# Kernel optimization log

Measured on AMD Instinct MI355X. Metric: run time of the kernel, lower is better.

The kernel has to match this reference:

```python
import jax, jax.numpy as jnp
import numpy as np

NUM_TOKENS = 8192
SEQ_LEN = 128
BATCH = 8192
INIT_SCALE = 0.02


def setup_inputs() -> dict:
    key = jax.random.key(0)
    k1, k2, k3, k4 = jax.random.split(key, 4)
    return {
        "rx_real": jax.random.normal(k1, (BATCH, SEQ_LEN), dtype=jnp.float32),
        "rx_imag": jax.random.normal(k2, (BATCH, SEQ_LEN), dtype=jnp.float32),
        "freq_real": jax.random.normal(k3, (NUM_TOKENS, SEQ_LEN), dtype=jnp.float32) * INIT_SCALE,
        "freq_imag": jax.random.normal(k4, (NUM_TOKENS, SEQ_LEN), dtype=jnp.float32) * INIT_SCALE,
        "temperature": jnp.asarray(1.0, dtype=jnp.float32),
    }


def reference(rx_real, rx_imag, freq_real, freq_imag, temperature):
    # Build complex waveform bank: ifft of learned frequency-domain params (ortho norm)
    freq = freq_real + 1j * freq_imag                      # [T, L] complex64
    bank = jnp.fft.ifft(freq, axis=-1, norm="ortho")       # [T, L] complex64

    rx = rx_real + 1j * rx_imag                            # [B, L] complex64

    # 'dot' similarity: complex GEMM against conjugated bank, then squared magnitude
    score = rx @ jnp.conj(bank).T                          # [B, T] complex64
    sim = score.real ** 2 + score.imag ** 2                # [B, T] float32

    # temperature scaling (use_temperature=True)
    return sim / temperature
```

## Files before the change

kernel.cpp:

```cpp
#include <hip/hip_runtime.h>
#include <stdint.h>


#define T_TOKENS 8192
#define B_BATCH  8192
#define L_SEQ    128
#define KDIM     256

typedef __bf16 bf16x8 __attribute__((ext_vector_type(8)));
typedef float  f32x4  __attribute__((ext_vector_type(4)));
typedef unsigned int u32x4 __attribute__((ext_vector_type(4)));

__device__ __forceinline__ unsigned short f2bf(float f) {
  unsigned int u = __builtin_bit_cast(unsigned int, f);
  u += 0x7FFFu + ((u >> 16) & 1u);
  return (unsigned short)(u >> 16);
}

__global__ void build_bank_kernel(const float* __restrict__ fr,
                                  const float* __restrict__ fi,
                                  unsigned int* __restrict__ B2) {
  __shared__ float  sfr[L_SEQ], sfi[L_SEQ];
  __shared__ float2 stw[L_SEQ];
  const int t = blockIdx.x, l = threadIdx.x;
  sfr[l] = fr[t * L_SEQ + l];
  sfi[l] = fi[t * L_SEQ + l];
  float sn, cs;
  __sincosf(6.283185307179586f * (float)l * (1.0f / 128.0f), &sn, &cs);
  stw[l] = make_float2(cs, sn);
  __syncthreads();
  float br = 0.f, bi = 0.f;
#pragma unroll 8
  for (int k = 0; k < L_SEQ; ++k) {
    const float2 tw = stw[(k * l) & 127];
    const float xr = sfr[k], xi = sfi[k];
    br = fmaf(xr, tw.x, br); br = fmaf(-xi, tw.y, br);
    bi = fmaf(xr, tw.y, bi); bi = fmaf(xi, tw.x, bi);
  }
  const float sc = 0.08838834764831845f;
  const unsigned int lo = f2bf(br * sc);
  const unsigned int hi = f2bf(bi * sc);
  B2[t * L_SEQ + l] = lo | (hi << 16);
}

__global__ void build_a_kernel(const float* __restrict__ rr,
                               const float* __restrict__ ri,
                               unsigned int* __restrict__ A2) {
  const int i = blockIdx.x * 256 + threadIdx.x;
  const unsigned int lo = f2bf(rr[i]);
  const unsigned int hi = f2bf(ri[i]);
  A2[i] = lo | (hi << 16);
}

typedef const __attribute__((address_space(1))) unsigned int* gas_u32p;
typedef __attribute__((address_space(3))) unsigned int* las_u32p;

__device__ __forceinline__ void gl_lds16(const void* g, void* l) {
  __builtin_amdgcn_global_load_lds((gas_u32p)g, (las_u32p)l, 16, 0, 0);
}

__device__ __forceinline__ bf16x8 make_imag(bf16x8 a) {
  u32x4 u = __builtin_bit_cast(u32x4, a);
#pragma unroll
  for (int i = 0; i < 4; ++i)
    u[i] = ((u[i] >> 16) | (u[i] << 16)) ^ 0x80000000u;
  return __builtin_bit_cast(bf16x8, u);
}

__global__ __launch_bounds__(256, 2) void gemm_kernel(
    const unsigned short* __restrict__ A2,
    const unsigned short* __restrict__ B2,
    const float* __restrict__ temp,
    float* __restrict__ out) {
  __shared__ __align__(16) unsigned short sA[2][128 * 64];
  __shared__ __align__(16) unsigned short sB[2][128 * 64];

  const int tid  = threadIdx.x;
  const int lane = tid & 63;
  const int wid  = tid >> 6;

  const int bid  = blockIdx.x;
  const int swz  = (bid & 7) * 512 + (bid >> 3);
  const int brow = swz >> 6;
  const int bcol = swz & 63;
  const int wr = wid >> 1, wc = wid & 1;

  const unsigned short* Abase = A2 + (size_t)brow * 128 * KDIM;
  const unsigned short* Bbase = B2 + (size_t)bcol * 128 * KDIM;

  f32x4 accre[4][4], accim[4][4];
#pragma unroll
  for (int m = 0; m < 4; ++m)
#pragma unroll
    for (int n = 0; n < 4; ++n) {
      accre[m][n] = f32x4{0.f, 0.f, 0.f, 0.f};
      accim[m][n] = f32x4{0.f, 0.f, 0.f, 0.f};
    }

  auto stage = [&](int ks, int buf) {
#pragma unroll
    for (int q = 0; q < 4; ++q) {
      const int unit = (q * 4 + wid) * 64 + lane;
      const int r = unit >> 3;
      const int c = (unit & 7) << 3;
      gl_lds16(Abase + (size_t)r * KDIM + ks * 64 + c,
               (char*)&sA[buf][0] + (size_t)(q * 4 + wid) * 1024);
      gl_lds16(Bbase + (size_t)r * KDIM + ks * 64 + c,
               (char*)&sB[buf][0] + (size_t)(q * 4 + wid) * 1024);
    }
  };

  stage(0, 0);

#pragma unroll
  for (int ks = 0; ks < 4; ++ks) {
    const int buf = ks & 1;
    __syncthreads();
    if (ks < 3) stage(ks + 1, buf ^ 1);

    const unsigned short* aptr =
        &sA[buf][(wr * 64 + (lane & 15)) * 64 + ((lane >> 4) << 3)];
    const unsigned short* bptr =
        &sB[buf][(wc * 64 + (lane & 15)) * 64 + ((lane >> 4) << 3)];
#pragma unroll
    for (int kk = 0; kk < 2; ++kk) {
      bf16x8 a[4], b[4];
#pragma unroll
      for (int m = 0; m < 4; ++m)
        a[m] = *(const bf16x8*)(aptr + m * 16 * 64 + kk * 32);
#pragma unroll
      for (int n = 0; n < 4; ++n)
        b[n] = *(const bf16x8*)(bptr + n * 16 * 64 + kk * 32);
#pragma unroll
      for (int m = 0; m < 4; ++m) {
        const bf16x8 ai = make_imag(a[m]);
#pragma unroll
        for (int n = 0; n < 4; ++n) {
          accre[m][n] = __builtin_amdgcn_mfma_f32_16x16x32_bf16(
              a[m], b[n], accre[m][n], 0, 0, 0);
          accim[m][n] = __builtin_amdgcn_mfma_f32_16x16x32_bf16(
              ai, b[n], accim[m][n], 0, 0, 0);
        }
      }
    }
  }

  const float inv_t = 1.0f / temp[0];
  const int r0 = brow * 128 + wr * 64 + ((lane >> 4) << 2);
  const int c0 = bcol * 128 + wc * 64 + (lane & 15);
#pragma unroll
  for (int m = 0; m < 4; ++m) {
#pragma unroll
    for (int n = 0; n < 4; ++n) {
      const f32x4 re = accre[m][n];
      const f32x4 im = accim[m][n];
#pragma unroll
      for (int j = 0; j < 4; ++j) {
        out[(size_t)(r0 + m * 16 + j) * T_TOKENS + (c0 + n * 16)] =
            (re[j] * re[j] + im[j] * im[j]) * inv_t;
      }
    }
  }
}

extern "C" void kernel_launch(void* const* d_in, const int* in_sizes, int n_in,
                              void* d_out, int out_size, void* d_ws, size_t ws_size,
                              hipStream_t stream) {
  const float* rx_r = (const float*)d_in[0];
  const float* rx_i = (const float*)d_in[1];
  const float* fq_r = (const float*)d_in[2];
  const float* fq_i = (const float*)d_in[3];
  const float* temp = (const float*)d_in[4];
  float* out = (float*)d_out;

  unsigned int* B2 = (unsigned int*)d_ws;
  unsigned int* A2 = (unsigned int*)((char*)d_ws + (4u << 20));

  build_bank_kernel<<<T_TOKENS, L_SEQ, 0, stream>>>(fq_r, fq_i, B2);
  build_a_kernel<<<(B_BATCH * L_SEQ) / 256, 256, 0, stream>>>(rx_r, rx_i, A2);
  gemm_kernel<<<(B_BATCH / 128) * (T_TOKENS / 128), 256, 0, stream>>>(
      (const unsigned short*)A2, (const unsigned short*)B2, temp, out);
}
```

Before: 123.9 us.

## Enlarge GEMM tile to 256x128 with 4-slot LDS pipeline and swizzle

```diff
diff --git a/kernel.cpp b/kernel.cpp
--- a/kernel.cpp
+++ b/kernel.cpp
@@ -5,7 +5,9 @@
 #define T_TOKENS 8192
 #define B_BATCH  8192
 #define L_SEQ    128
-#define KDIM     256
+
+#define SLOT_BYTES 24576
+#define SB_OFF     16384
 
 typedef __bf16 bf16x8 __attribute__((ext_vector_type(8)));
 typedef float  f32x4  __attribute__((ext_vector_type(4)));
@@ -52,11 +54,10 @@
   A2[i] = lo | (hi << 16);
 }
 
-typedef const __attribute__((address_space(1))) unsigned int* gas_u32p;
-typedef __attribute__((address_space(3))) unsigned int* las_u32p;
-
-__device__ __forceinline__ void gl_lds16(const void* g, void* l) {
-  __builtin_amdgcn_global_load_lds((gas_u32p)g, (las_u32p)l, 16, 0, 0);
+__device__ __forceinline__ void gl_lds16(const char* g, char* l) {
+  __builtin_amdgcn_global_load_lds(
+      (const __attribute__((address_space(1))) unsigned int*)g,
+      (__attribute__((address_space(3))) unsigned int*)l, 16, 0, 0);
 }
 
 __device__ __forceinline__ bf16x8 make_imag(bf16x8 a) {
@@ -67,26 +68,46 @@
   return __builtin_bit_cast(bf16x8, u);
 }
 
-__global__ __launch_bounds__(256, 2) void gemm_kernel(
-    const unsigned short* __restrict__ A2,
-    const unsigned short* __restrict__ B2,
-    const float* __restrict__ temp,
-    float* __restrict__ out) {
-  __shared__ __align__(16) unsigned short sA[2][128 * 64];
-  __shared__ __align__(16) unsigned short sB[2][128 * 64];
-
+__device__ __forceinline__ int swz4(int row) { return ((row + (row >> 2)) & 3) << 4; }
+
+extern __shared__ __align__(16) char smem[];
+
+__global__ __launch_bounds__(512, 1) void gemm_kernel(
+    const char* __restrict__ A2, const char* __restrict__ B2,
+    const float* __restrict__ temp, float* __restrict__ out) {
   const int tid  = threadIdx.x;
   const int lane = tid & 63;
   const int wid  = tid >> 6;
 
+  const float inv_t = 1.0f / temp[0];
+  asm volatile("" :: "v"(inv_t));
+
   const int bid  = blockIdx.x;
-  const int swz  = (bid & 7) * 512 + (bid >> 3);
+  const int swz  = (bid & 7) * 256 + (bid >> 3);
   const int brow = swz >> 6;
   const int bcol = swz & 63;
   const int wr = wid >> 1, wc = wid & 1;
 
-  const unsigned short* Abase = A2 + (size_t)brow * 128 * KDIM;
-  const unsigned short* Bbase = B2 + (size_t)bcol * 128 * KDIM;
+  const int l4 = lane >> 2, lm = lane & 3;
+  const int rowA0 = wid * 32 + l4;
+  const int rowA1 = rowA0 + 16;
+  const int rowB  = wid * 16 + l4;
+  const char* gA0 = A2 + (size_t)(brow * 256 + rowA0) * 512 + ((lm * 16) ^ swz4(rowA0));
+  const char* gA1 = A2 + (size_t)(brow * 256 + rowA1) * 512 + ((lm * 16) ^ swz4(rowA1));
+  const char* gB  = B2 + (size_t)(bcol * 128 + rowB ) * 512 + ((lm * 16) ^ swz4(rowB));
+
+  int offA[4], offB[4];
+  const int cb = (lane >> 4) * 16;
+#pragma unroll
+  for (int m = 0; m < 4; ++m) {
+    const int r = wr * 64 + m * 16 + (lane & 15);
+    offA[m] = r * 64 + (cb ^ swz4(r));
+  }
+#pragma unroll
+  for (int n = 0; n < 4; ++n) {
+    const int r = wc * 64 + n * 16 + (lane & 15);
+    offB[n] = SB_OFF + r * 64 + (cb ^ swz4(r));
+  }
 
   f32x4 accre[4][4], accim[4][4];
 #pragma unroll
@@ -97,56 +118,65 @@
       accim[m][n] = f32x4{0.f, 0.f, 0.f, 0.f};
     }
 
-  auto stage = [&](int ks, int buf) {
-#pragma unroll
-    for (int q = 0; q < 4; ++q) {
-      const int unit = (q * 4 + wid) * 64 + lane;
-      const int r = unit >> 3;
-      const int c = (unit & 7) << 3;
-      gl_lds16(Abase + (size_t)r * KDIM + ks * 64 + c,
-               (char*)&sA[buf][0] + (size_t)(q * 4 + wid) * 1024);
-      gl_lds16(Bbase + (size_t)r * KDIM + ks * 64 + c,
-               (char*)&sB[buf][0] + (size_t)(q * 4 + wid) * 1024);
-    }
-  };
-
-  stage(0, 0);
-
-#pragma unroll
-  for (int ks = 0; ks < 4; ++ks) {
-    const int buf = ks & 1;
-    __syncthreads();
-    if (ks < 3) stage(ks + 1, buf ^ 1);
-
-    const unsigned short* aptr =
-        &sA[buf][(wr * 64 + (lane & 15)) * 64 + ((lane >> 4) << 3)];
-    const unsigned short* bptr =
-        &sB[buf][(wc * 64 + (lane & 15)) * 64 + ((lane >> 4) << 3)];
-#pragma unroll
-    for (int kk = 0; kk < 2; ++kk) {
-      bf16x8 a[4], b[4];
-#pragma unroll
-      for (int m = 0; m < 4; ++m)
-        a[m] = *(const bf16x8*)(aptr + m * 16 * 64 + kk * 32);
-#pragma unroll
-      for (int n = 0; n < 4; ++n)
-        b[n] = *(const bf16x8*)(bptr + n * 16 * 64 + kk * 32);
-#pragma unroll
-      for (int m = 0; m < 4; ++m) {
-        const bf16x8 ai = make_imag(a[m]);
-#pragma unroll
-        for (int n = 0; n < 4; ++n) {
-          accre[m][n] = __builtin_amdgcn_mfma_f32_16x16x32_bf16(
-              a[m], b[n], accre[m][n], 0, 0, 0);
-          accim[m][n] = __builtin_amdgcn_mfma_f32_16x16x32_bf16(
-              ai, b[n], accim[m][n], 0, 0, 0);
-        }
-      }
-    }
-  }
-
-  const float inv_t = 1.0f / temp[0];
-  const int r0 = brow * 128 + wr * 64 + ((lane >> 4) << 2);
+#define STAGE(KC) do {                                                     \
+    char* sl_ = smem + ((KC) & 3) * SLOT_BYTES;                            \
+    int koff_ = (KC) * 64;                                                 \
+    asm("" : "+v"(koff_));                                                 \
+    gl_lds16(gA0 + koff_, sl_ + wid * 2048);                               \
+    gl_lds16(gA1 + koff_, sl_ + wid * 2048 + 1024);                        \
+    gl_lds16(gB  + koff_, sl_ + SB_OFF + wid * 1024);                      \
+  } while (0)
+
+#define FENCE asm volatile("" ::: "memory")
+
+#define PHASE(C, VM, DOSTAGE) do {                                         \
+    const char* slb_ = smem + ((C) & 3) * SLOT_BYTES;                      \
+    bf16x8 a_[4], b_[4];                                                   \
+    _Pragma("unroll") for (int m = 0; m < 4; ++m)                          \
+      a_[m] = *(const bf16x8*)(slb_ + offA[m]);                            \
+    _Pragma("unroll") for (int n = 0; n < 4; ++n)                          \
+      b_[n] = *(const bf16x8*)(slb_ + offB[n]);                            \
+    if (DOSTAGE) { STAGE((C) + 3); }                                       \
+    if ((VM) == 4)      asm volatile("s_waitcnt vmcnt(4)" ::: "memory");   \
+    else if ((VM) == 3) asm volatile("s_waitcnt vmcnt(3)" ::: "memory");   \
+    else if ((VM) == 0) asm volatile("s_waitcnt vmcnt(0)" ::: "memory");   \
+    __builtin_amdgcn_s_barrier();                                          \
+    asm volatile("s_waitcnt lgkmcnt(0)" ::: "memory");                     \
+    __builtin_amdgcn_s_setprio(1);                                         \
+    _Pragma("unroll") for (int m = 0; m < 4; ++m) {                        \
+      const bf16x8 ai_ = make_imag(a_[m]);                                 \
+      _Pragma("unroll") for (int n = 0; n < 4; ++n) {                      \
+        accre[m][n] = __builtin_amdgcn_mfma_f32_16x16x32_bf16(             \
+            a_[m], b_[n], accre[m][n], 0, 0, 0);                           \
+        accim[m][n] = __builtin_amdgcn_mfma_f32_16x16x32_bf16(             \
+            ai_, b_[n], accim[m][n], 0, 0, 0);                             \
+      }                                                                    \
+    }                                                                      \
+    __builtin_amdgcn_s_setprio(0);                                         \
+    __builtin_amdgcn_s_barrier();                                          \
+    FENCE;                                                                 \
+  } while (0)
+
+  asm volatile("s_waitcnt vmcnt(0) lgkmcnt(0)" ::: "memory");
+
+  STAGE(0); STAGE(1); STAGE(2);
+  asm volatile("s_waitcnt vmcnt(4)" ::: "memory");
+  __builtin_amdgcn_s_barrier();
+  FENCE;
+
+  PHASE(0, 4, 1);
+  PHASE(1, 4, 1);
+  PHASE(2, 4, 1);
+  PHASE(3, 4, 1);
+  PHASE(4, 4, 1);
+  PHASE(5, 3, 0);
+  PHASE(6, 0, 0);
+  PHASE(7, -1, 0);
+
+#undef PHASE
+#undef STAGE
+
+  const int r0 = brow * 256 + wr * 64 + ((lane >> 4) << 2);
   const int c0 = bcol * 128 + wc * 64 + (lane & 15);
 #pragma unroll
   for (int m = 0; m < 4; ++m) {
@@ -176,8 +206,11 @@
   unsigned int* B2 = (unsigned int*)d_ws;
   unsigned int* A2 = (unsigned int*)((char*)d_ws + (4u << 20));
 
+  (void)hipFuncSetAttribute((const void*)gemm_kernel,
+                            hipFuncAttributeMaxDynamicSharedMemorySize, 98304);
+
   build_bank_kernel<<<T_TOKENS, L_SEQ, 0, stream>>>(fq_r, fq_i, B2);
   build_a_kernel<<<(B_BATCH * L_SEQ) / 256, 256, 0, stream>>>(rx_r, rx_i, A2);
-  gemm_kernel<<<(B_BATCH / 128) * (T_TOKENS / 128), 256, 0, stream>>>(
-      (const unsigned short*)A2, (const unsigned short*)B2, temp, out);
-}
+  gemm_kernel<<<(B_BATCH / 256) * (T_TOKENS / 128), 512, 98304, stream>>>(
+      (const char*)A2, (const char*)B2, temp, out);
+}
```

New measurement: 130.3 us. 5.1% more time.

## Keep bank tile in registers and stream A rows directly without LDS

Applied to the files above, without the earlier changes.

```diff
diff --git a/kernel.cpp b/kernel.cpp
--- a/kernel.cpp
+++ b/kernel.cpp
@@ -5,7 +5,6 @@
 #define T_TOKENS 8192
 #define B_BATCH  8192
 #define L_SEQ    128
-#define KDIM     256
 
 typedef __bf16 bf16x8 __attribute__((ext_vector_type(8)));
 typedef float  f32x4  __attribute__((ext_vector_type(4)));
@@ -52,13 +51,6 @@
   A2[i] = lo | (hi << 16);
 }
 
-typedef const __attribute__((address_space(1))) unsigned int* gas_u32p;
-typedef __attribute__((address_space(3))) unsigned int* las_u32p;
-
-__device__ __forceinline__ void gl_lds16(const void* g, void* l) {
-  __builtin_amdgcn_global_load_lds((gas_u32p)g, (las_u32p)l, 16, 0, 0);
-}
-
 __device__ __forceinline__ bf16x8 make_imag(bf16x8 a) {
   u32x4 u = __builtin_bit_cast(u32x4, a);
 #pragma unroll
@@ -67,97 +59,91 @@
   return __builtin_bit_cast(bf16x8, u);
 }
 
-__global__ __launch_bounds__(256, 2) void gemm_kernel(
-    const unsigned short* __restrict__ A2,
-    const unsigned short* __restrict__ B2,
-    const float* __restrict__ temp,
-    float* __restrict__ out) {
-  __shared__ __align__(16) unsigned short sA[2][128 * 64];
-  __shared__ __align__(16) unsigned short sB[2][128 * 64];
-
+__global__ __launch_bounds__(256, 3) void gemm_kernel(
+    const char* __restrict__ A2, const char* __restrict__ B2,
+    const float* __restrict__ temp, float* __restrict__ out) {
   const int tid  = threadIdx.x;
   const int lane = tid & 63;
   const int wid  = tid >> 6;
+  const float inv_t = 1.0f / temp[0];
 
   const int bid  = blockIdx.x;
-  const int swz  = (bid & 7) * 512 + (bid >> 3);
-  const int brow = swz >> 6;
-  const int bcol = swz & 63;
-  const int wr = wid >> 1, wc = wid & 1;
+  const int g    = bid & 7;
+  const int nblk = bid >> 3;
 
-  const unsigned short* Abase = A2 + (size_t)brow * 128 * KDIM;
-  const unsigned short* Bbase = B2 + (size_t)bcol * 128 * KDIM;
+  const int lrow = lane & 15;
+  const int lk16 = (lane >> 4) * 16;
 
-  f32x4 accre[4][4], accim[4][4];
+  bf16x8 br[8][2];
+  {
+    const char* bb = B2 + (size_t)(nblk * 32 + lrow) * 512 + lk16;
 #pragma unroll
-  for (int m = 0; m < 4; ++m)
+    for (int kc = 0; kc < 8; ++kc) {
 #pragma unroll
-    for (int n = 0; n < 4; ++n) {
+      for (int n = 0; n < 2; ++n)
+        br[kc][n] = *(const bf16x8*)(bb + (size_t)n * 16 * 512 + kc * 64);
+    }
+  }
+
+  const size_t aoff0 = (size_t)lrow * 512 + lk16;
+  const size_t aoff1 = aoff0 + 16 * 512;
+  const char* pA = A2 + ((size_t)g * 1024 + wid * 32) * 512;
+
+  f32x4 accre[2][2], accim[2][2];
+#pragma unroll
+  for (int m = 0; m < 2; ++m)
+#pragma unroll
+    for (int n = 0; n < 2; ++n) {
       accre[m][n] = f32x4{0.f, 0.f, 0.f, 0.f};
       accim[m][n] = f32x4{0.f, 0.f, 0.f, 0.f};
     }
 
-  auto stage = [&](int ks, int buf) {
+  bf16x8 ar[4][2];
 #pragma unroll
-    for (int q = 0; q < 4; ++q) {
-      const int unit = (q * 4 + wid) * 64 + lane;
-      const int r = unit >> 3;
-      const int c = (unit & 7) << 3;
-      gl_lds16(Abase + (size_t)r * KDIM + ks * 64 + c,
-               (char*)&sA[buf][0] + (size_t)(q * 4 + wid) * 1024);
-      gl_lds16(Bbase + (size_t)r * KDIM + ks * 64 + c,
-               (char*)&sB[buf][0] + (size_t)(q * 4 + wid) * 1024);
-    }
-  };
-
-  stage(0, 0);
-
-#pragma unroll
-  for (int ks = 0; ks < 4; ++ks) {
-    const int buf = ks & 1;
-    __syncthreads();
-    if (ks < 3) stage(ks + 1, buf ^ 1);
-
-    const unsigned short* aptr =
-        &sA[buf][(wr * 64 + (lane & 15)) * 64 + ((lane >> 4) << 3)];
-    const unsigned short* bptr =
-        &sB[buf][(wc * 64 + (lane & 15)) * 64 + ((lane >> 4) << 3)];
-#pragma unroll
-    for (int kk = 0; kk < 2; ++kk) {
-      bf16x8 a[4], b[4];
-#pragma unroll
-      for (int m = 0; m < 4; ++m)
-        a[m] = *(const bf16x8*)(aptr + m * 16 * 64 + kk * 32);
-#pragma unroll
-      for (int n = 0; n < 4; ++n)
-        b[n] = *(const bf16x8*)(bptr + n * 16 * 64 + kk * 32);
-#pragma unroll
-      for (int m = 0; m < 4; ++m) {
-        const bf16x8 ai = make_imag(a[m]);
-#pragma unroll
-        for (int n = 0; n < 4; ++n) {
-          accre[m][n] = __builtin_amdgcn_mfma_f32_16x16x32_bf16(
-              a[m], b[n], accre[m][n], 0, 0, 0);
-          accim[m][n] = __builtin_amdgcn_mfma_f32_16x16x32_bf16(
-              ai, b[n], accim[m][n], 0, 0, 0);
-        }
-      }
-    }
+  for (int kc = 0; kc < 4; ++kc) {
+    ar[kc][0] = *(const bf16x8*)(pA + aoff0 + kc * 64);
+    ar[kc][1] = *(const bf16x8*)(pA + aoff1 + kc * 64);
   }
 
-  const float inv_t = 1.0f / temp[0];
-  const int r0 = brow * 128 + wr * 64 + ((lane >> 4) << 2);
-  const int c0 = bcol * 128 + wc * 64 + (lane & 15);
+  for (int t = 0; t < 8; ++t) {
+    const char* pcur  = pA + (size_t)t * 128 * 512;
+    const char* pnext = (t == 7) ? pcur : pcur + 128 * 512;
+
+#define PH(KC, PS, KS) do {                                                  \
+    const bf16x8 a0 = ar[(KC) & 3][0], a1 = ar[(KC) & 3][1];                 \
+    ar[(KC) & 3][0] = *(const bf16x8*)((PS) + aoff0 + (KS) * 64);            \
+    ar[(KC) & 3][1] = *(const bf16x8*)((PS) + aoff1 + (KS) * 64);            \
+    const bf16x8 ai0 = make_imag(a0), ai1 = make_imag(a1);                   \
+    accre[0][0] = __builtin_amdgcn_mfma_f32_16x16x32_bf16(a0, br[KC][0], accre[0][0], 0, 0, 0); \
+    accim[0][0] = __builtin_amdgcn_mfma_f32_16x16x32_bf16(ai0, br[KC][0], accim[0][0], 0, 0, 0); \
+    accre[0][1] = __builtin_amdgcn_mfma_f32_16x16x32_bf16(a0, br[KC][1], accre[0][1], 0, 0, 0); \
+    accim[0][1] = __builtin_amdgcn_mfma_f32_16x16x32_bf16(ai0, br[KC][1], accim[0][1], 0, 0, 0); \
+    accre[1][0] = __builtin_amdgcn_mfma_f32_16x16x32_bf16(a1, br[KC][0], accre[1][0], 0, 0, 0); \
+    accim[1][0] = __builtin_amdgcn_mfma_f32_16x16x32_bf16(ai1, br[KC][0], accim[1][0], 0, 0, 0); \
+    accre[1][1] = __builtin_amdgcn_mfma_f32_16x16x32_bf16(a1, br[KC][1], accre[1][1], 0, 0, 0); \
+    accim[1][1] = __builtin_amdgcn_mfma_f32_16x16x32_bf16(ai1, br[KC][1], accim[1][1], 0, 0, 0); \
+  } while (0)
+
+    PH(0, pcur, 4);  PH(1, pcur, 5);  PH(2, pcur, 6);  PH(3, pcur, 7);
+    PH(4, pnext, 0); PH(5, pnext, 1); PH(6, pnext, 2); PH(7, pnext, 3);
+#undef PH
+
+    const int r0 = g * 1024 + t * 128 + wid * 32 + ((lane >> 4) << 2);
+    const int c0 = nblk * 32 + lrow;
 #pragma unroll
-  for (int m = 0; m < 4; ++m) {
+    for (int m = 0; m < 2; ++m) {
 #pragma unroll
-    for (int n = 0; n < 4; ++n) {
-      const f32x4 re = accre[m][n];
-      const f32x4 im = accim[m][n];
+      for (int n = 0; n < 2; ++n) {
+        const f32x4 re = accre[m][n];
+        const f32x4 im = accim[m][n];
 #pragma unroll
-      for (int j = 0; j < 4; ++j) {
-        out[(size_t)(r0 + m * 16 + j) * T_TOKENS + (c0 + n * 16)] =
-            (re[j] * re[j] + im[j] * im[j]) * inv_t;
+        for (int j = 0; j < 4; ++j) {
+          __builtin_nontemporal_store(
+              (re[j] * re[j] + im[j] * im[j]) * inv_t,
+              &out[(size_t)(r0 + m * 16 + j) * T_TOKENS + (c0 + n * 16)]);
+        }
+        accre[m][n] = f32x4{0.f, 0.f, 0.f, 0.f};
+        accim[m][n] = f32x4{0.f, 0.f, 0.f, 0.f};
       }
     }
   }
@@ -178,6 +164,6 @@
 
   build_bank_kernel<<<T_TOKENS, L_SEQ, 0, stream>>>(fq_r, fq_i, B2);
   build_a_kernel<<<(B_BATCH * L_SEQ) / 256, 256, 0, stream>>>(rx_r, rx_i, A2);
-  gemm_kernel<<<(B_BATCH / 128) * (T_TOKENS / 128), 256, 0, stream>>>(
-      (const unsigned short*)A2, (const unsigned short*)B2, temp, out);
+  gemm_kernel<<<8 * (T_TOKENS / 32), 256, 0, stream>>>(
+      (const char*)A2, (const char*)B2, temp, out);
 }
```

Measured after the change: 175.0 us. +41.3%, slower.
